# Kernel tuning notes

Hardware: AMD Instinct MI355X
Metric: run time of the kernel (lower is better)

The kernel has to match this reference:

```python
import jax, jax.numpy as jnp
import numpy as np

B, L, D, DFF, MODES = 16, 1536, 512, 2048, 64
KERNELS = (3, 5, 7)


def setup_inputs() -> dict:
    key = jax.random.key(0)
    ks = jax.random.split(key, 12)
    scale = 1.0 / (D * D)
    f32 = jnp.float32
    return {
        "x": jax.random.normal(ks[0], (B, L, D), f32),
        "w_real": scale * jax.random.normal(ks[1], (D, D, MODES), f32),
        "w_imag": scale * jax.random.normal(ks[2], (D, D, MODES), f32),
        "conv1_w": jax.random.normal(ks[3], (DFF, D), f32) / np.sqrt(D).astype(np.float32),
        "conv2_w": jax.random.normal(ks[4], (D, DFF), f32) / np.sqrt(DFF).astype(np.float32),
        "d1_w1": jax.random.normal(ks[5], (D // 2, D), f32) / np.sqrt(D).astype(np.float32),
        "d1_b1": jnp.zeros((D // 2,), f32),
        "d1_w2": jax.random.normal(ks[6], (len(KERNELS), D // 2), f32) / np.sqrt(D // 2).astype(np.float32),
        "d1_b2": jnp.zeros((len(KERNELS),), f32),
        "d2_w1": jax.random.normal(ks[7], (D // 2, D), f32) / np.sqrt(D).astype(np.float32),
        "d2_b1": jnp.zeros((D // 2,), f32),
        "d2_w2": jax.random.normal(ks[8], (len(KERNELS), D // 2), f32) / np.sqrt(D // 2).astype(np.float32),
        "d2_b2": jnp.zeros((len(KERNELS),), f32),
    }


def _avg_pool1d(x, k):
    # torch AvgPool1d(kernel=k, stride=1, padding=k//2), count_include_pad=True:
    # zero-pad then divide by k everywhere. x: (B, L, D) -> (B, L, D) for odd k.
    pad = k // 2
    xp = jnp.pad(x, ((0, 0), (pad, pad), (0, 0)))
    cs = jnp.pad(jnp.cumsum(xp, axis=1), ((0, 0), (1, 0), (0, 0)))
    return (cs[:, k:, :] - cs[:, :-k, :]) / k


def _moe_decomp(x, w1, b1, w2, b2):
    # trends: (B, L, D, E)
    trends = jnp.stack([_avg_pool1d(x, k) for k in KERNELS], axis=-1)
    h = jax.nn.relu(jnp.einsum("bld,hd->blh", x, w1) + b1)
    logits = jnp.einsum("blh,eh->ble", h, w2) + b2
    gates = jax.nn.softmax(logits, axis=-1)[:, :, None, :]  # (B, L, 1, E)
    x_trend = jnp.sum(trends * gates, axis=-1)
    return x - x_trend  # seasonal component


def _fourier_block(x, w_real, w_imag):
    q_ft = jnp.fft.rfft(x, axis=1)  # (B, L//2+1, D) complex
    modes = min(MODES, q_ft.shape[1])
    weights = (w_real + 1j * w_imag).astype(jnp.complex64)  # (D, D, modes)
    # batched complex matmul over the kept modes (fuses the per-mode loop)
    out_m = jnp.einsum("bmd,dem->bme", q_ft[:, :modes, :], weights[:, :, :modes])
    out_ft = jnp.zeros((x.shape[0], x.shape[1] // 2 + 1, x.shape[2]), jnp.complex64)
    out_ft = out_ft.at[:, :modes, :].set(out_m)
    return jnp.fft.irfft(out_ft, n=x.shape[1], axis=1)


def reference(x, w_real, w_imag, conv1_w, conv2_w,
              d1_w1, d1_b1, d1_w2, d1_b2,
              d2_w1, d2_b1, d2_w2, d2_b2):
    # FEB-f + residual (dropout = identity in eval)
    x = x + _fourier_block(x, w_real, w_imag)
    x = _moe_decomp(x, d1_w1, d1_b1, d1_w2, d1_b2)
    # 1x1 conv FFN == per-token linear layers
    y = jax.nn.relu(jnp.einsum("bld,fd->blf", x, conv1_w))
    y = jnp.einsum("blf,df->bld", y, conv2_w)
    res = _moe_decomp(x + y, d2_w1, d2_b1, d2_w2, d2_b2)
    return res
```

## Files before the change

kernel.cpp:

```cpp
#include <hip/hip_runtime.h>

#define B_   16
#define L_   1536
#define D_   512
#define DFF_ 2048
#define NM   64
#define HID  256

typedef short short8  __attribute__((ext_vector_type(8)));
typedef short short4v __attribute__((ext_vector_type(4)));
typedef float f32x4   __attribute__((ext_vector_type(4)));

__device__ __forceinline__ float b2f(short s) {
  unsigned int u = ((unsigned int)(unsigned short)s) << 16;
  float f; __builtin_memcpy(&f, &u, 4); return f;
}
__device__ __forceinline__ short f2b(float f) {
  unsigned int u; __builtin_memcpy(&u, &f, 4);
  u += 0x7fffu + ((u >> 16) & 1u);
  return (short)(u >> 16);
}
__device__ __forceinline__ f32x4 zero4() {
  f32x4 v; v[0]=0.f; v[1]=0.f; v[2]=0.f; v[3]=0.f; return v;
}

#define MFMA(a,b,c) __builtin_amdgcn_mfma_f32_16x16x32_bf16((a),(b),(c),0,0,0)
#define SWZ(row, grp) (((row) << 6) + ((((grp) ^ ((row) & 7))) << 3))
#define GLDS16(gp, lp) __builtin_amdgcn_global_load_lds( \
    (const __attribute__((address_space(1))) void*)(gp), \
    (__attribute__((address_space(3))) void*)(lp), 16, 0, 0)
#define MEMFENCE asm volatile("" ::: "memory")

__device__ __forceinline__ unsigned ldsaddr(const void* p) {
  return (unsigned)(unsigned long long)(const __attribute__((address_space(3))) void*)p;
}
__device__ __forceinline__ short8 dsr128(unsigned a) {
  short8 r;
  asm volatile("ds_read_b128 %0, %1" : "=v"(r) : "v"(a));
  return r;
}

__global__ __launch_bounds__(256) void zero_out(float* __restrict__ o, int n) {
  int i = blockIdx.x * 256 + threadIdx.x;
  if (i < n) o[i] = 0.f;
}

__global__ __launch_bounds__(256) void prep_all(
    const float* __restrict__ conv1_w, const float* __restrict__ conv2_w,
    const float* __restrict__ d1_w1,  const float* __restrict__ d2_w1,
    short* __restrict__ c1, short* __restrict__ c2,
    short* __restrict__ dw1, short* __restrict__ dw2,
    short* __restrict__ tcs, short* __restrict__ basis)
{
  int blk = blockIdx.x;
  if (blk < 2304) {
    const float* s; short* d; int i;
    if (blk < 1024)      { s = conv1_w; d = c1;  i = blk * 256 + threadIdx.x; }
    else if (blk < 2048) { s = conv2_w; d = c2;  i = (blk - 1024) * 256 + threadIdx.x; }
    else if (blk < 2176) { s = d1_w1;   d = dw1; i = (blk - 2048) * 256 + threadIdx.x; }
    else                 { s = d2_w1;   d = dw2; i = (blk - 2176) * 256 + threadIdx.x; }
    f32x4 v = ((const f32x4*)s)[i];
    short4v o;
    #pragma unroll
    for (int j = 0; j < 4; ++j) o[j] = f2b(v[j]);
    ((short4v*)d)[i] = o;
    return;
  }
  if (blk < 3072) {
    int i = (blk - 2304) * 256 + threadIdx.x;
    int m = i / L_, l = i - m * L_;
    int mm = (m < 64) ? m : (m - 64);
    int r = (mm * l) % L_;
    float th = (float)r * (6.283185307179586f / (float)L_);
    float s, c; __sincosf(th, &s, &c);
    tcs[i] = f2b((m < 64) ? c : -s);
    return;
  }
  {
    int i = (blk - 3072) * 256 + threadIdx.x;
    int l = i >> 7, k = i & 127;
    int m = (k < 64) ? k : (k - 64);
    int r = (m * l) % L_;
    float th = (float)r * (6.283185307179586f / (float)L_);
    float s, c; __sincosf(th, &s, &c);
    float v = (k < 64) ? ((m == 0) ? 1.f : 2.f) * (1.f / (float)L_) * c
                       : (-2.f / (float)L_) * s;
    basis[i] = f2b(v);
  }
}

__global__ __launch_bounds__(256) void transpose_w(
    const float* __restrict__ wre, const float* __restrict__ wim,
    short* __restrict__ wtr, short* __restrict__ wti)
{
  __shared__ float tile[64][17];
  int dc = blockIdx.x, e = blockIdx.y, t = threadIdx.x;
  int zz = blockIdx.z;
  const float* w = (zz < 4) ? wre : wim;
  short* wt      = (zz < 4) ? wtr : wti;
  int mBase = (zz & 3) * 16;
  {
    int dl = t >> 2, mg = t & 3;
    f32x4 v = *(const f32x4*)(w + ((long)(dc * 64 + dl) * 512 + e) * 64 + mBase + mg * 4);
    tile[dl][mg*4+0] = v[0]; tile[dl][mg*4+1] = v[1];
    tile[dl][mg*4+2] = v[2]; tile[dl][mg*4+3] = v[3];
  }
  __syncthreads();
  if (t < 128) {
    int mr = t >> 3, dg = t & 7;
    short8 o;
    #pragma unroll
    for (int j = 0; j < 8; ++j) o[j] = f2b(tile[dg * 8 + j][mr]);
    *(short8*)(wt + ((long)(mBase + mr) * 512 + e) * 512 + dc * 64 + dg * 8) = o;
  }
}

__global__ __launch_bounds__(256) void transpose_x(const float* __restrict__ x,
                                                   short* __restrict__ xt) {
  __shared__ float tile[64][65];
  int dc = blockIdx.x, lc = blockIdx.y, b = blockIdx.z, t = threadIdx.x;
  const float* xb = x + (long)b * L_ * D_;
  #pragma unroll
  for (int i = 0; i < 4; ++i) {
    int idx = i * 256 + t; int ll = idx >> 4, dg = idx & 15;
    f32x4 v = *(const f32x4*)(xb + (long)(lc * 64 + ll) * D_ + dc * 64 + dg * 4);
    tile[ll][dg*4+0] = v[0]; tile[ll][dg*4+1] = v[1];
    tile[ll][dg*4+2] = v[2]; tile[ll][dg*4+3] = v[3];
  }
  __syncthreads();
  #pragma unroll
  for (int i = 0; i < 2; ++i) {
    int idx = i * 256 + t; int dl = idx >> 3, lg = idx & 7;
    short8 o;
    #pragma unroll
    for (int j = 0; j < 8; ++j) o[j] = f2b(tile[lg * 8 + j][dl]);
    *(short8*)(xt + ((long)b * D_ + dc * 64 + dl) * L_ + lc * 64 + lg * 8) = o;
  }
}

template<bool RELU, bool HASBIAS>
__global__ __launch_bounds__(256) void gemm64(
    const short* __restrict__ A, long ldA,
    const short* __restrict__ W, long ldW,
    const float* __restrict__ bias,
    short* __restrict__ outB, long csr, long csc, int K)
{
  __shared__ short lA[2][64 * 64];
  __shared__ short lW[2][64 * 64];
  const int t = threadIdx.x, lane = t & 63, wid = t >> 6;
  const int quad = lane >> 4, l15 = lane & 15;
  const int wm = (wid & 1) * 32, wn = (wid >> 1) * 32;
  const long row0 = (long)blockIdx.x * 64, col0 = (long)blockIdx.y * 64;
  const short* Ab = A + row0 * ldA;
  const short* Wb = W + col0 * ldW;

  int srcrow[2]; long srcoff[2];
  #pragma unroll
  for (int i = 0; i < 2; ++i) {
    int c = wid * 2 + i;
    int r = c * 8 + (lane >> 3);
    int g = (lane & 7) ^ (r & 7);
    srcrow[i] = r; srcoff[i] = g * 8;
  }

  f32x4 acc[2][2];
  #pragma unroll
  for (int i = 0; i < 2; ++i)
    #pragma unroll
    for (int j = 0; j < 2; ++j) acc[i][j] = zero4();

  const int nk = K >> 6;
  #pragma unroll
  for (int i = 0; i < 2; ++i) {
    int c = wid * 2 + i;
    GLDS16(Ab + (long)srcrow[i] * ldA + srcoff[i], lA[0] + c * 512);
    GLDS16(Wb + (long)srcrow[i] * ldW + srcoff[i], lW[0] + c * 512);
  }
  if (nk > 1) {
    #pragma unroll
    for (int i = 0; i < 2; ++i) {
      int c = wid * 2 + i;
      GLDS16(Ab + (long)srcrow[i] * ldA + 64 + srcoff[i], lA[1] + c * 512);
      GLDS16(Wb + (long)srcrow[i] * ldW + 64 + srcoff[i], lW[1] + c * 512);
    }
  }

  for (int it = 0; it < nk; ++it) {
    if (it + 1 < nk) asm volatile("s_waitcnt vmcnt(4)" ::: "memory");
    else             asm volatile("s_waitcnt vmcnt(0)" ::: "memory");
    __builtin_amdgcn_s_barrier();
    const int cur = it & 1;
    const short* bufA = lA[cur];
    const short* bufW = lW[cur];
    #pragma unroll
    for (int ks = 0; ks < 2; ++ks) {
      int gq = ks * 4 + quad;
      short8 a0 = *(const short8*)&bufA[SWZ(wm + l15, gq)];
      short8 a1 = *(const short8*)&bufA[SWZ(wm + 16 + l15, gq)];
      short8 b0 = *(const short8*)&bufW[SWZ(wn + l15, gq)];
      short8 b1 = *(const short8*)&bufW[SWZ(wn + 16 + l15, gq)];
      acc[0][0] = MFMA(a0, b0, acc[0][0]);
      acc[0][1] = MFMA(a0, b1, acc[0][1]);
      acc[1][0] = MFMA(a1, b0, acc[1][0]);
      acc[1][1] = MFMA(a1, b1, acc[1][1]);
    }
    asm volatile("s_waitcnt lgkmcnt(0)" ::: "memory");
    __builtin_amdgcn_s_barrier();
    const long kn = (long)(it + 2) * 64;
    if (kn < K) {
      #pragma unroll
      for (int i = 0; i < 2; ++i) {
        int c = wid * 2 + i;
        GLDS16(Ab + (long)srcrow[i] * ldA + kn + srcoff[i], lA[cur] + c * 512);
        GLDS16(Wb + (long)srcrow[i] * ldW + kn + srcoff[i], lW[cur] + c * 512);
      }
    }
  }

  #pragma unroll
  for (int ni = 0; ni < 2; ++ni) {
    long col = col0 + wn + ni * 16 + l15;
    float bvv = HASBIAS ? bias[col] : 0.f;
    #pragma unroll
    for (int mi = 0; mi < 2; ++mi) {
      #pragma unroll
      for (int r = 0; r < 4; ++r) {
        long row = row0 + wm + mi * 16 + quad * 4 + r;
        float v = acc[mi][ni][r];
        if (HASBIAS) v += bvv;
        if (RELU)    v = fmaxf(v, 0.f);
        outB[row * csr + col * csc] = f2b(v);
      }
    }
  }
}

template<bool RELU, bool HASBIAS, bool HASRES, bool RESB>
__global__ __launch_bounds__(256) void gemm128(
    const short* __restrict__ A, long ldA, long Az,
    const short* __restrict__ W, long ldW, long Wz,
    const float* __restrict__ bias,
    const void* __restrict__ res, long ldres, long resZ,
    short* __restrict__ outB, long ldC, long Cz, int K)
{
  __shared__ short lA[2][128 * 64];
  __shared__ short lW[2][128 * 64];
  const int t = threadIdx.x, lane = t & 63, wid = t >> 6;
  const int quad = lane >> 4, l15 = lane & 15;
  const int wm = (wid & 1) * 64, wn = (wid >> 1) * 64;
  const long row0 = (long)blockIdx.x * 128, col0 = (long)blockIdx.y * 128;
  const int z = blockIdx.z;
  const short* Ab = A + (long)z * Az + row0 * ldA;
  const short* Wb = W + (long)z * Wz + col0 * ldW;

  int srcrow[4]; long srcoff[4];
  #pragma unroll
  for (int i = 0; i < 4; ++i) {
    int c = wid * 4 + i;
    int r = c * 8 + (lane >> 3);
    int g = (lane & 7) ^ (r & 7);
    srcrow[i] = r; srcoff[i] = g * 8;
  }

  f32x4 acc[4][4];
  #pragma unroll
  for (int i = 0; i < 4; ++i)
    #pragma unroll
    for (int j = 0; j < 4; ++j) acc[i][j] = zero4();

  const int nk = K >> 6;
  #pragma unroll
  for (int i = 0; i < 4; ++i) {
    int c = wid * 4 + i;
    GLDS16(Ab + (long)srcrow[i] * ldA + srcoff[i], lA[0] + c * 512);
    GLDS16(Wb + (long)srcrow[i] * ldW + srcoff[i], lW[0] + c * 512);
  }
  if (nk > 1) {
    #pragma unroll
    for (int i = 0; i < 4; ++i) {
      int c = wid * 4 + i;
      GLDS16(Ab + (long)srcrow[i] * ldA + 64 + srcoff[i], lA[1] + c * 512);
      GLDS16(Wb + (long)srcrow[i] * ldW + 64 + srcoff[i], lW[1] + c * 512);
    }
  }

  for (int it = 0; it < nk; ++it) {
    if (it + 1 < nk) asm volatile("s_waitcnt vmcnt(8)" ::: "memory");
    else             asm volatile("s_waitcnt vmcnt(0)" ::: "memory");
    __builtin_amdgcn_s_barrier();
    const int cur = it & 1;
    const short* bufA = lA[cur];
    const short* bufW = lW[cur];
    #pragma unroll
    for (int ks = 0; ks < 2; ++ks) {
      int gq = ks * 4 + quad;
      short8 av[4], bv[4];
      #pragma unroll
      for (int mi = 0; mi < 4; ++mi) av[mi] = *(const short8*)&bufA[SWZ(wm + mi * 16 + l15, gq)];
      #pragma unroll
      for (int ni = 0; ni < 4; ++ni) bv[ni] = *(const short8*)&bufW[SWZ(wn + ni * 16 + l15, gq)];
      #pragma unroll
      for (int mi = 0; mi < 4; ++mi)
        #pragma unroll
        for (int ni = 0; ni < 4; ++ni)
          acc[mi][ni] = MFMA(av[mi], bv[ni], acc[mi][ni]);
    }
    asm volatile("s_waitcnt lgkmcnt(0)" ::: "memory");
    __builtin_amdgcn_s_barrier();
    const long kn = (long)(it + 2) * 64;
    if (kn < K) {
      #pragma unroll
      for (int i = 0; i < 4; ++i) {
        int c = wid * 4 + i;
        GLDS16(Ab + (long)srcrow[i] * ldA + kn + srcoff[i], lA[cur] + c * 512);
        GLDS16(Wb + (long)srcrow[i] * ldW + kn + srcoff[i], lW[cur] + c * 512);
      }
    }
  }

  #pragma unroll
  for (int ni = 0; ni < 4; ++ni) {
    long col = col0 + wn + ni * 16 + l15;
    float bvv = HASBIAS ? bias[col] : 0.f;
    #pragma unroll
    for (int mi = 0; mi < 4; ++mi) {
      #pragma unroll
      for (int r = 0; r < 4; ++r) {
        long row = row0 + wm + mi * 16 + quad * 4 + r;
        float v = acc[mi][ni][r];
        if (HASBIAS) v += bvv;
        if (RELU)    v = fmaxf(v, 0.f);
        if (HASRES) {
          long ro = (long)z * resZ + row * ldres + col;
          v += RESB ? b2f(((const short*)res)[ro]) : ((const float*)res)[ro];
        }
        outB[(long)z * Cz + row * ldC + col] = f2b(v);
      }
    }
  }
}

template<bool RELU, bool HASRES>
__global__ __launch_bounds__(512, 2) void gemm256(
    const short* __restrict__ A, long ldA,
    const short* __restrict__ W, long ldW,
    const short* __restrict__ res, long ldres,
    short* __restrict__ outB, long ldC, int K, int gn)
{
  __shared__ short sh[65536];
  const int t = threadIdx.x;
  const int lane = t & 63, wid = t >> 6;
  const int quad = lane >> 4, l15 = lane & 15;
  const int wr = wid >> 2, wc = wid & 3;
  const int wch = wc >> 1, cbw = (wc & 1) * 64;

  const int nwg = gridDim.x, cpx = nwg >> 3;
  const int wg = (blockIdx.x & 7) * cpx + (blockIdx.x >> 3);
  const int bx = wg / gn, by = wg - bx * gn;
  const long row0 = (long)bx * 256, col0 = (long)by * 256;
  const short* Ab = A + row0 * ldA;
  const short* Wb = W + col0 * ldW;

  const int srw = t >> 3;
  const int sg  = (t & 7) ^ (srw & 7);

#define STAGE(TP, KB) do {                                                   \
    const long ko_ = (long)(KB) + sg * 8;                                    \
    _Pragma("unroll")                                                        \
    for (int h_ = 0; h_ < 2; ++h_) {                                         \
      short* dA_ = sh + ((TP) * 2 + h_) * 8192;                              \
      short* dB_ = sh + 32768 + ((TP) * 2 + h_) * 8192;                      \
      _Pragma("unroll")                                                      \
      for (int j_ = 0; j_ < 2; ++j_) {                                       \
        const long gr_ = (long)(h_ * 128 + srw + j_ * 64);                   \
        GLDS16(Ab + gr_ * ldA + ko_, dA_ + (j_ * 512 + t) * 8);              \
        GLDS16(Wb + gr_ * ldW + ko_, dB_ + (j_ * 512 + t) * 8);              \
      }                                                                      \
    }                                                                        \
  } while (0)

  const unsigned shb  = ldsaddr(sh);
  const unsigned swz0 = (unsigned)((quad ^ (l15 & 7)) << 4);
  const unsigned swz1 = swz0 ^ 64u;
  const unsigned aB = shb + wr * 16384u + (unsigned)(l15 * 128);
  const unsigned bB = shb + 65536u + wch * 16384u + (unsigned)((cbw + l15) * 128);

  f32x4 acc[8][4];
  #pragma unroll
  for (int i = 0; i < 8; ++i)
    #pragma unroll
    for (int j = 0; j < 4; ++j) acc[i][j] = zero4();

  const int NK = K >> 6;
  STAGE(0, 0);

  for (int i = 0; i < NK; ++i) {
    const unsigned tpo = (unsigned)(i & 1) * 32768u;
    if (i + 1 < NK) {
      STAGE((i + 1) & 1, (i + 1) << 6);
      asm volatile("s_waitcnt vmcnt(8)" ::: "memory");
    } else {
      asm volatile("s_waitcnt vmcnt(0)" ::: "memory");
    }
    __builtin_amdgcn_s_barrier();
    __builtin_amdgcn_sched_barrier(0);

    short8 bv[4][2], a0[4][2], a1[4][2];
    #pragma unroll
    for (int ni = 0; ni < 4; ++ni) {
      bv[ni][0] = dsr128(bB + tpo + ni * 2048u + swz0);
      bv[ni][1] = dsr128(bB + tpo + ni * 2048u + swz1);
    }
    #pragma unroll
    for (int u = 0; u < 4; ++u) {
      a0[u][0] = dsr128(aB + tpo + u * 2048u + swz0);
      a0[u][1] = dsr128(aB + tpo + u * 2048u + swz1);
    }
    #pragma unroll
    for (int u = 0; u < 4; ++u) {
      a1[u][0] = dsr128(aB + tpo + 8192u + u * 2048u + swz0);
      a1[u][1] = dsr128(aB + tpo + 8192u + u * 2048u + swz1);
    }
    asm volatile("s_waitcnt lgkmcnt(8)" ::: "memory");
    __builtin_amdgcn_sched_barrier(0);
    __builtin_amdgcn_s_setprio(1);
    #pragma unroll
    for (int ks = 0; ks < 2; ++ks)
      #pragma unroll
      for (int u = 0; u < 4; ++u)
        #pragma unroll
        for (int ni = 0; ni < 4; ++ni)
          acc[u][ni] = MFMA(a0[u][ks], bv[ni][ks], acc[u][ni]);
    __builtin_amdgcn_s_setprio(0);
    asm volatile("s_waitcnt lgkmcnt(0)" ::: "memory");
    __builtin_amdgcn_sched_barrier(0);
    __builtin_amdgcn_s_setprio(1);
    #pragma unroll
    for (int ks = 0; ks < 2; ++ks)
      #pragma unroll
      for (int u = 0; u < 4; ++u)
        #pragma unroll
        for (int ni = 0; ni < 4; ++ni)
          acc[4 + u][ni] = MFMA(a1[u][ks], bv[ni][ks], acc[4 + u][ni]);
    __builtin_amdgcn_s_setprio(0);
    __builtin_amdgcn_sched_barrier(0);
    __builtin_amdgcn_s_barrier();
  }

  #pragma unroll
  for (int ni = 0; ni < 4; ++ni) {
    long col = col0 + wc * 64 + ni * 16 + l15;
    #pragma unroll
    for (int mi = 0; mi < 8; ++mi) {
      #pragma unroll
      for (int r = 0; r < 4; ++r) {
        long row = row0 + wr * 128 + mi * 16 + quad * 4 + r;
        float v = acc[mi][ni][r];
        if (RELU) v = fmaxf(v, 0.f);
        if (HASRES) v += b2f(res[row * ldres + col]);
        outB[row * ldC + col] = f2b(v);
      }
    }
  }
#undef STAGE
}

__global__ __launch_bounds__(256) void mode_gemm(
    const short* __restrict__ qr, const short* __restrict__ qi,
    const short* __restrict__ wr, const short* __restrict__ wi,
    short* __restrict__ outm)
{
  __shared__ short lqr[16 * 64], lqi[16 * 64], lwr[64 * 64], lwi[64 * 64];
  const int m = blockIdx.x, en = blockIdx.y;
  const int t = threadIdx.x, lane = t & 63, wid = t >> 6;
  const int quad = lane >> 4, l15 = lane & 15;
  const short* qrb = qr + (long)m * (B_ * D_);
  const short* qib = qi + (long)m * (B_ * D_);
  const short* wrb = wr + (long)m * (D_ * D_) + (long)en * 64 * D_;
  const short* wib = wi + (long)m * (D_ * D_) + (long)en * 64 * D_;
  f32x4 accr = zero4(), acci = zero4();
  for (int k0 = 0; k0 < D_; k0 += 64) {
    __syncthreads();
    {
      int idx = t & 127; int r = idx >> 3, cg = idx & 7;
      const short* src = (t < 128 ? qrb : qib) + r * D_ + k0 + cg * 8;
      short* dst = (t < 128) ? lqr : lqi;
      *(short8*)&dst[SWZ(r, cg)] = *(const short8*)src;
    }
    #pragma unroll
    for (int i = 0; i < 4; ++i) {
      int idx = i * 256 + t;
      int which = idx >> 9, idx2 = idx & 511;
      int r = idx2 >> 3, cg = idx2 & 7;
      const short* src = (which ? wib : wrb) + r * D_ + k0 + cg * 8;
      short* dst = which ? lwi : lwr;
      *(short8*)&dst[SWZ(r, cg)] = *(const short8*)src;
    }
    __syncthreads();
    #pragma unroll
    for (int ks = 0; ks < 2; ++ks) {
      int gq = ks * 4 + quad;
      short8 ar = *(const short8*)&lqr[SWZ(l15, gq)];
      short8 ai = *(const short8*)&lqi[SWZ(l15, gq)];
      short8 br = *(const short8*)&lwr[SWZ(wid * 16 + l15, gq)];
      short8 bi = *(const short8*)&lwi[SWZ(wid * 16 + l15, gq)];
      short8 nai;
      #pragma unroll
      for (int j = 0; j < 8; ++j) nai[j] = (short)(ai[j] ^ (short)0x8000);
      accr = MFMA(ar, br, accr);
      accr = MFMA(nai, bi, accr);
      acci = MFMA(ar, bi, acci);
      acci = MFMA(ai, br, acci);
    }
  }
  #pragma unroll
  for (int r = 0; r < 4; ++r) {
    int bb = quad * 4 + r;
    long e = (long)en * 64 + wid * 16 + l15;
    long base = ((long)bb * D_ + e) * 128 + m;
    outm[base]      = f2b(accr[r]);
    outm[base + 64] = f2b(acci[r]);
  }
}

template<bool OUTF, bool WRITEB>
__global__ __launch_bounds__(512) void combine_kernel(
    const short* __restrict__ xin, const short* __restrict__ h,
    const float* __restrict__ w2, const float* __restrict__ b2,
    float* __restrict__ outf, short* __restrict__ outb)
{
  __shared__ float lG[64][4];
  int lc = blockIdx.x, b = blockIdx.y, t = threadIdx.x;
  int wid = t >> 6, lane = t & 63;
  int l0 = lc * 64;
  #pragma unroll
  for (int pi = 0; pi < 8; ++pi) {
    int pos = wid * 8 + pi;
    long row = (long)b * L_ + l0 + pos;
    short4v hh = *(const short4v*)(h + row * HID + lane * 4);
    float hv[4];
    #pragma unroll
    for (int j = 0; j < 4; ++j) hv[j] = b2f(hh[j]);
    float lg[3];
    #pragma unroll
    for (int e = 0; e < 3; ++e) {
      const float* wrow = w2 + e * HID + lane * 4;
      float p = hv[0] * wrow[0] + hv[1] * wrow[1] + hv[2] * wrow[2] + hv[3] * wrow[3];
      #pragma unroll
      for (int off = 32; off >= 1; off >>= 1) p += __shfl_xor(p, off);
      lg[e] = p + b2[e];
    }
    float mx = fmaxf(lg[0], fmaxf(lg[1], lg[2]));
    float e0 = __expf(lg[0] - mx), e1 = __expf(lg[1] - mx), e2 = __expf(lg[2] - mx);
    float inv = 1.f / (e0 + e1 + e2);
    float gv = (lane == 0) ? e0 * inv : (lane == 1) ? e1 * inv : e2 * inv;
    if (lane < 3) lG[pos][lane] = gv;
  }
  __syncthreads();

  int d = t;
  const short* xb = xin + (long)b * L_ * D_ + d;
  float win[7];
  #pragma unroll
  for (int j = 0; j < 6; ++j) {
    int l = l0 - 3 + j;
    win[j] = (l >= 0 && l < L_) ? b2f(xb[(long)l * D_]) : 0.f;
  }
  for (int i = 0; i < 64; ++i) {
    int lcn = l0 + i;
    int lr = lcn + 3;
    win[6] = (lr < L_) ? b2f(xb[(long)lr * D_]) : 0.f;
    float s3 = win[2] + win[3] + win[4];
    float s5 = s3 + win[1] + win[5];
    float s7 = s5 + win[0] + win[6];
    float trend = lG[i][0] * s3 * (1.f / 3.f) + lG[i][1] * s5 * (1.f / 5.f)
                + lG[i][2] * s7 * (1.f / 7.f);
    float v = win[3] - trend;
    long o = ((long)b * L_ + lcn) * D_ + d;
    if (OUTF)   outf[o] = v;
    if (WRITEB) outb[o] = f2b(v);
    #pragma unroll
    for (int j = 0; j < 6; ++j) win[j] = win[j + 1];
  }
}

extern "C" void kernel_launch(void* const* d_in, const int* in_sizes, int n_in,
                              void* d_out, int out_size, void* d_ws, size_t ws_size,
                              hipStream_t stream) {
  const float* x       = (const float*)d_in[0];
  const float* w_real  = (const float*)d_in[1];
  const float* w_imag  = (const float*)d_in[2];
  const float* conv1_w = (const float*)d_in[3];
  const float* conv2_w = (const float*)d_in[4];
  const float* d1_w1   = (const float*)d_in[5];
  const float* d1_b1   = (const float*)d_in[6];
  const float* d1_w2   = (const float*)d_in[7];
  const float* d1_b2   = (const float*)d_in[8];
  const float* d2_w1   = (const float*)d_in[9];
  const float* d2_b1   = (const float*)d_in[10];
  const float* d2_w2   = (const float*)d_in[11];
  const float* d2_b2   = (const float*)d_in[12];
  float* OUT = (float*)d_out;

  const size_t REQ_BIG = 144703488, REQ_SMALL = 98566144;
  if (ws_size < REQ_SMALL) {
    zero_out<<<(out_size + 255) / 256, 256, 0, stream>>>(OUT, out_size);
    return;
  }
  const bool big = (ws_size >= REQ_BIG);

  char* ws = (char*)d_ws;
  short* C1WB  = (short*)(ws + 0);
  short* C2WB  = (short*)(ws + 2097152);
  short* D1W1B = (short*)(ws + 4194304);
  short* D2W1B = (short*)(ws + 4456448);
  short* TCS   = (short*)(ws + 4718592);
  short* BASIS = (short*)(ws + 5111808);
  short* XT    = (short*)(ws + 6291456);
  short* Y1    = XT;
  short* QRI   = (short*)(ws + 31457280);
  short* OUTM  = (short*)(ws + 33554432);
  short* WTR   = (short*)(ws + 35651584);
  short* X1B   = WTR;
  short* WTI   = (short*)(ws + 69206016);
  short* X2B   = (short*)(ws + (big ? 106954752 : 60817408));
  short* H     = (short*)(ws + (big ? 132120576 : 85983232));

  prep_all<<<3840, 256, 0, stream>>>(conv1_w, conv2_w, d1_w1, d2_w1,
                                     C1WB, C2WB, D1W1B, D2W1B, TCS, BASIS);
  transpose_w<<<dim3(8, 512, 8), 256, 0, stream>>>(w_real, w_imag, WTR, WTI);
  transpose_x<<<dim3(8, 24, 16), 256, 0, stream>>>(x, XT);

  gemm64<false, false><<<dim3(128, 2), 256, 0, stream>>>(
      XT, L_, TCS, L_, nullptr, QRI, 1, (long)B_ * D_, L_);

  mode_gemm<<<dim3(64, 8), 256, 0, stream>>>(QRI, QRI + 64 * B_ * D_, WTR, WTI, OUTM);

  gemm128<false, false, true, false><<<dim3(12, 4, 16), 256, 0, stream>>>(
      BASIS, 128, 0, OUTM, 128, (long)D_ * 128, nullptr,
      x, D_, (long)L_ * D_, X1B, D_, (long)L_ * D_, 128);

  gemm64<true, true><<<dim3(384, 4), 256, 0, stream>>>(
      X1B, D_, D1W1B, D_, d1_b1, H, HID, 1, D_);
  combine_kernel<false, true><<<dim3(24, 16), 512, 0, stream>>>(
      X1B, H, d1_w2, d1_b2, nullptr, X2B);

  {
    const int nchunk = big ? 1 : 2;
    const long rows = big ? 24576 : 12288;
    const int gm = (int)(rows / 256);
    for (int rc = 0; rc < nchunk; ++rc) {
      short* Ain = X2B + (long)rc * rows * D_;
      gemm256<true, false><<<dim3(gm * (DFF_ / 256)), 512, 0, stream>>>(
          Ain, D_, C1WB, D_, nullptr, 0, Y1, DFF_, D_, DFF_ / 256);
      gemm256<false, true><<<dim3(gm * (D_ / 256)), 512, 0, stream>>>(
          Y1, DFF_, C2WB, DFF_, Ain, D_, Ain, D_, DFF_, D_ / 256);
    }
  }

  gemm64<true, true><<<dim3(384, 4), 256, 0, stream>>>(
      X2B, D_, D2W1B, D_, d2_b1, H, HID, 1, D_);
  combine_kernel<true, false><<<dim3(24, 16), 512, 0, stream>>>(
      X2B, H, d2_w2, d2_b2, OUT, nullptr);
}
```

Before: 582.9 us.

## Template FFN GEMM on row tile and pipeline LDS reads with MFMA

Generalizes the 256x256 FFN GEMM into a template over the row-tile height and changes the warp layout so each warp covers 64 full columns. The inner loop now reads A fragments in pairs while earlier MFMA groups run, using partial lgkmcnt waits to overlap LDS reads with matrix math. The second FFN GEMM (K=2048, N=512) uses a 192-row tile to produce more workgroups and better fill the CUs. The trade-off is less reuse per tile, plus a finer wait/schedule sequence that needs correct counter values.

Measured after the change: 567.2 us. 2.7% less time.

```diff
diff --git a/kernel.cpp b/kernel.cpp
--- a/kernel.cpp
+++ b/kernel.cpp
@@ -30,6 +30,9 @@
     (const __attribute__((address_space(1))) void*)(gp), \
     (__attribute__((address_space(3))) void*)(lp), 16, 0, 0)
 #define MEMFENCE asm volatile("" ::: "memory")
+#define SB0 __builtin_amdgcn_sched_barrier(0)
+#define LGKM4 asm volatile("s_waitcnt lgkmcnt(4)" ::: "memory")
+#define LGKM0 asm volatile("s_waitcnt lgkmcnt(0)" ::: "memory")
 
 __device__ __forceinline__ unsigned ldsaddr(const void* p) {
   return (unsigned)(unsigned long long)(const __attribute__((address_space(3))) void*)p;
@@ -340,24 +343,25 @@
   }
 }
 
-template<bool RELU, bool HASRES>
-__global__ __launch_bounds__(512, 2) void gemm256(
+template<int BM, bool RELU, bool HASRES>
+__global__ __launch_bounds__(512, 2) void gemmT(
     const short* __restrict__ A, long ldA,
     const short* __restrict__ W, long ldW,
     const short* __restrict__ res, long ldres,
     short* __restrict__ outB, long ldC, int K, int gn)
 {
-  __shared__ short sh[65536];
+  constexpr int MF   = BM / 32;
+  constexpr int ALD  = BM / 64;
+  __shared__ short sh[BM * 128 + 32768];
   const int t = threadIdx.x;
   const int lane = t & 63, wid = t >> 6;
   const int quad = lane >> 4, l15 = lane & 15;
   const int wr = wid >> 2, wc = wid & 3;
-  const int wch = wc >> 1, cbw = (wc & 1) * 64;
 
   const int nwg = gridDim.x, cpx = nwg >> 3;
   const int wg = (blockIdx.x & 7) * cpx + (blockIdx.x >> 3);
   const int bx = wg / gn, by = wg - bx * gn;
-  const long row0 = (long)bx * 256, col0 = (long)by * 256;
+  const long row0 = (long)bx * BM, col0 = (long)by * 256;
   const short* Ab = A + row0 * ldA;
   const short* Wb = W + col0 * ldW;
 
@@ -366,28 +370,47 @@
 
 #define STAGE(TP, KB) do {                                                   \
     const long ko_ = (long)(KB) + sg * 8;                                    \
+    short* dA_ = sh + (TP) * (BM * 64);                                      \
+    short* dB_ = sh + BM * 128 + (TP) * 16384;                               \
     _Pragma("unroll")                                                        \
-    for (int h_ = 0; h_ < 2; ++h_) {                                         \
-      short* dA_ = sh + ((TP) * 2 + h_) * 8192;                              \
-      short* dB_ = sh + 32768 + ((TP) * 2 + h_) * 8192;                      \
-      _Pragma("unroll")                                                      \
-      for (int j_ = 0; j_ < 2; ++j_) {                                       \
-        const long gr_ = (long)(h_ * 128 + srw + j_ * 64);                   \
-        GLDS16(Ab + gr_ * ldA + ko_, dA_ + (j_ * 512 + t) * 8);              \
-        GLDS16(Wb + gr_ * ldW + ko_, dB_ + (j_ * 512 + t) * 8);              \
-      }                                                                      \
-    }                                                                        \
+    for (int ld = 0; ld < ALD; ++ld)                                         \
+      GLDS16(Ab + (long)(ld * 64 + srw) * ldA + ko_, dA_ + (ld * 512 + t) * 8); \
+    _Pragma("unroll")                                                        \
+    for (int ld = 0; ld < 4; ++ld)                                           \
+      GLDS16(Wb + (long)(ld * 64 + srw) * ldW + ko_, dB_ + (ld * 512 + t) * 8); \
+  } while (0)
+#define WAITV() do {                                                         \
+    if constexpr (BM == 256) asm volatile("s_waitcnt vmcnt(8)" ::: "memory");\
+    else                     asm volatile("s_waitcnt vmcnt(7)" ::: "memory");\
   } while (0)
 
   const unsigned shb  = ldsaddr(sh);
   const unsigned swz0 = (unsigned)((quad ^ (l15 & 7)) << 4);
   const unsigned swz1 = swz0 ^ 64u;
-  const unsigned aB = shb + wr * 16384u + (unsigned)(l15 * 128);
-  const unsigned bB = shb + 65536u + wch * 16384u + (unsigned)((cbw + l15) * 128);
-
-  f32x4 acc[8][4];
-  #pragma unroll
-  for (int i = 0; i < 8; ++i)
+  const unsigned aBs = shb + (unsigned)(wr * (BM / 2) * 128) + (unsigned)(l15 * 128);
+  const unsigned bBs = shb + (unsigned)(BM * 256) + (unsigned)((wc * 64 + l15) * 128);
+
+#define RDP(BUF, AO, P) do {                                                 \
+    BUF[0][0] = dsr128(aBs + (AO) + ((P) * 2 + 0) * 2048u + swz0);           \
+    BUF[0][1] = dsr128(aBs + (AO) + ((P) * 2 + 0) * 2048u + swz1);           \
+    BUF[1][0] = dsr128(aBs + (AO) + ((P) * 2 + 1) * 2048u + swz0);           \
+    BUF[1][1] = dsr128(aBs + (AO) + ((P) * 2 + 1) * 2048u + swz1);           \
+  } while (0)
+#define MMAP(P, BUF) do {                                                    \
+    __builtin_amdgcn_s_setprio(1);                                           \
+    _Pragma("unroll")                                                        \
+    for (int ks = 0; ks < 2; ++ks)                                           \
+      _Pragma("unroll")                                                      \
+      for (int u = 0; u < 2; ++u)                                            \
+        _Pragma("unroll")                                                    \
+        for (int ni = 0; ni < 4; ++ni)                                       \
+          acc[(P) * 2 + u][ni] = MFMA(BUF[u][ks], bv[ni][ks], acc[(P)*2+u][ni]); \
+    __builtin_amdgcn_s_setprio(0);                                           \
+  } while (0)
+
+  f32x4 acc[MF][4];
+  #pragma unroll
+  for (int i = 0; i < MF; ++i)
     #pragma unroll
     for (int j = 0; j < 4; ++j) acc[i][j] = zero4();
 
@@ -395,55 +418,41 @@
   STAGE(0, 0);
 
   for (int i = 0; i < NK; ++i) {
-    const unsigned tpo = (unsigned)(i & 1) * 32768u;
+    const unsigned ao = (unsigned)(i & 1) * (unsigned)(BM * 128);
+    const unsigned bo = (unsigned)(i & 1) * 32768u;
     if (i + 1 < NK) {
       STAGE((i + 1) & 1, (i + 1) << 6);
-      asm volatile("s_waitcnt vmcnt(8)" ::: "memory");
+      WAITV();
     } else {
       asm volatile("s_waitcnt vmcnt(0)" ::: "memory");
     }
     __builtin_amdgcn_s_barrier();
-    __builtin_amdgcn_sched_barrier(0);
-
-    short8 bv[4][2], a0[4][2], a1[4][2];
+    SB0;
+
+    short8 bv[4][2], Aa[2][2], Abf[2][2], Ac[2][2];
     #pragma unroll
     for (int ni = 0; ni < 4; ++ni) {
-      bv[ni][0] = dsr128(bB + tpo + ni * 2048u + swz0);
-      bv[ni][1] = dsr128(bB + tpo + ni * 2048u + swz1);
-    }
-    #pragma unroll
-    for (int u = 0; u < 4; ++u) {
-      a0[u][0] = dsr128(aB + tpo + u * 2048u + swz0);
-      a0[u][1] = dsr128(aB + tpo + u * 2048u + swz1);
-    }
-    #pragma unroll
-    for (int u = 0; u < 4; ++u) {
-      a1[u][0] = dsr128(aB + tpo + 8192u + u * 2048u + swz0);
-      a1[u][1] = dsr128(aB + tpo + 8192u + u * 2048u + swz1);
-    }
-    asm volatile("s_waitcnt lgkmcnt(8)" ::: "memory");
-    __builtin_amdgcn_sched_barrier(0);
-    __builtin_amdgcn_s_setprio(1);
-    #pragma unroll
-    for (int ks = 0; ks < 2; ++ks)
-      #pragma unroll
-      for (int u = 0; u < 4; ++u)
-        #pragma unroll
-        for (int ni = 0; ni < 4; ++ni)
-          acc[u][ni] = MFMA(a0[u][ks], bv[ni][ks], acc[u][ni]);
-    __builtin_amdgcn_s_setprio(0);
-    asm volatile("s_waitcnt lgkmcnt(0)" ::: "memory");
-    __builtin_amdgcn_sched_barrier(0);
-    __builtin_amdgcn_s_setprio(1);
-    #pragma unroll
-    for (int ks = 0; ks < 2; ++ks)
-      #pragma unroll
-      for (int u = 0; u < 4; ++u)
-        #pragma unroll
-        for (int ni = 0; ni < 4; ++ni)
-          acc[4 + u][ni] = MFMA(a1[u][ks], bv[ni][ks], acc[4 + u][ni]);
-    __builtin_amdgcn_s_setprio(0);
-    __builtin_amdgcn_sched_barrier(0);
+      bv[ni][0] = dsr128(bBs + bo + ni * 2048u + swz0);
+      bv[ni][1] = dsr128(bBs + bo + ni * 2048u + swz1);
+    }
+    RDP(Aa, ao, 0);
+    RDP(Abf, ao, 1);
+    LGKM4; SB0;
+    RDP(Ac, ao, 2);
+    MMAP(0, Aa);
+    LGKM4; SB0;
+    if constexpr (MF == 8) {
+      RDP(Aa, ao, 3);
+      MMAP(1, Abf);
+      LGKM4; SB0;
+      MMAP(2, Ac);
+      LGKM0; SB0;
+      MMAP(3, Aa);
+    } else {
+      MMAP(1, Abf);
+      LGKM0; SB0;
+      MMAP(2, Ac);
+    }
     __builtin_amdgcn_s_barrier();
   }
 
@@ -451,10 +460,10 @@
   for (int ni = 0; ni < 4; ++ni) {
     long col = col0 + wc * 64 + ni * 16 + l15;
     #pragma unroll
-    for (int mi = 0; mi < 8; ++mi) {
+    for (int mi = 0; mi < MF; ++mi) {
       #pragma unroll
       for (int r = 0; r < 4; ++r) {
-        long row = row0 + wr * 128 + mi * 16 + quad * 4 + r;
+        long row = row0 + wr * (BM / 2) + mi * 16 + quad * 4 + r;
         float v = acc[mi][ni][r];
         if (RELU) v = fmaxf(v, 0.f);
         if (HASRES) v += b2f(res[row * ldres + col]);
@@ -463,6 +472,9 @@
     }
   }
 #undef STAGE
+#undef WAITV
+#undef RDP
+#undef MMAP
 }
 
 __global__ __launch_bounds__(256) void mode_gemm(
@@ -648,12 +660,11 @@
   {
     const int nchunk = big ? 1 : 2;
     const long rows = big ? 24576 : 12288;
-    const int gm = (int)(rows / 256);
     for (int rc = 0; rc < nchunk; ++rc) {
       short* Ain = X2B + (long)rc * rows * D_;
-      gemm256<true, false><<<dim3(gm * (DFF_ / 256)), 512, 0, stream>>>(
+      gemmT<256, true, false><<<dim3((int)(rows / 256) * (DFF_ / 256)), 512, 0, stream>>>(
           Ain, D_, C1WB, D_, nullptr, 0, Y1, DFF_, D_, DFF_ / 256);
-      gemm256<false, true><<<dim3(gm * (D_ / 256)), 512, 0, stream>>>(
+      gemmT<192, false, true><<<dim3((int)(rows / 192) * (D_ / 256)), 512, 0, stream>>>(
           Y1, DFF_, C2WB, DFF_, Ain, D_, Ain, D_, DFF_, D_ / 256);
     }
   }
```
